# Kernel optimization log

Hardware: AMD Instinct MI355X
Metric: run time of the kernel (lower is better)

Reference implementation:

```python
import jax, jax.numpy as jnp
import numpy as np

K = 8               # top-k frequencies
PRED_LEN = 96       # prediction_length
LOW_FREQ = 1        # low_frequency cutoff (drops DC)


def setup_inputs() -> dict:
    key = jax.random.key(0)
    x = jax.random.normal(key, (32, 2048, 64), dtype=jnp.float32)
    return {"x": x}


def reference(x):
    b, t, d = x.shape
    x_freq = jnp.fft.rfft(x, axis=1)                 # (b, t//2+1, d) complex
    freqs = jnp.fft.rfftfreq(t).astype(x.dtype)
    if t % 2 == 0:
        x_freq = x_freq[:, LOW_FREQ:-1]              # drop DC and Nyquist
        f = freqs[LOW_FREQ:-1]
    else:
        x_freq = x_freq[:, LOW_FREQ:]
        f = freqs[LOW_FREQ:]

    # top-k over frequency dim (axis=1), independently per (b, d)
    mag = jnp.abs(x_freq)                            # (b, F, d)
    _, idx = jax.lax.top_k(jnp.moveaxis(mag, 1, 2), K)  # (b, d, K), sorted desc
    idx = jnp.moveaxis(idx, 1, 2)                    # (b, K, d)
    x_k = jnp.take_along_axis(x_freq, idx, axis=1)   # (b, K, d) complex
    f_k = f[idx]                                     # (b, K, d)

    # extrapolate: add conjugate (negative) frequencies, then cos-sum
    x2 = jnp.concatenate([x_k, jnp.conj(x_k)], axis=1)  # (b, 2K, d)
    f2 = jnp.concatenate([f_k, -f_k], axis=1)           # (b, 2K, d)
    t_val = jnp.arange(t + PRED_LEN, dtype=x.dtype)     # (T,)
    amp = jnp.abs(x2) / t                               # (b, 2K, d)
    phase = jnp.angle(x2)                               # (b, 2K, d)
    # (b, 2K, T, d) broadcast intermediate, reduced over freq axis
    x_time = amp[:, :, None, :] * jnp.cos(
        2.0 * np.float32(np.pi) * f2[:, :, None, :] * t_val[None, None, :, None]
        + phase[:, :, None, :]
    )
    return x_time.sum(axis=1)                        # (b, t+PRED_LEN, d)
```

## Files before the change

### kernel.cpp

```cpp
#include <hip/hip_runtime.h>
#include <math.h>

#define BB 32
#define TT 2048
#define DD 64
#define PRED 96
#define TP (TT + PRED)
#define KTOP 8
#define MARGIN 8e-4f
#define PI_D 3.14159265358979323846

__device__ __forceinline__ int br6(int l) { return (int)(__brev((unsigned)l) >> 26); }
static constexpr int BR3[8] = {0,4,2,6,1,5,3,7};
static constexpr float C32T[16] = {
    1.0f, 0.98078528040323044913f, 0.92387953251128675613f, 0.83146961230254523708f,
    0.70710678118654752440f, 0.55557023301960222474f, 0.38268343236508977173f, 0.19509032201612826785f,
    0.0f, -0.19509032201612826785f, -0.38268343236508977173f, -0.55557023301960222474f,
    -0.70710678118654752440f, -0.83146961230254523708f, -0.92387953251128675613f, -0.98078528040323044913f};
static constexpr float S32T[16] = {
    0.0f, 0.19509032201612826785f, 0.38268343236508977173f, 0.55557023301960222474f,
    0.70710678118654752440f, 0.83146961230254523708f, 0.92387953251128675613f, 0.98078528040323044913f,
    1.0f, 0.98078528040323044913f, 0.92387953251128675613f, 0.83146961230254523708f,
    0.70710678118654752440f, 0.55557023301960222474f, 0.38268343236508977173f, 0.19509032201612826785f};

__device__ __forceinline__ float2 ctw(float2 a, int m) {
    const float rev = (float)m * (1.0f / 2048.0f);
    const float c = __builtin_amdgcn_cosf(rev);
    const float s = __builtin_amdgcn_sinf(rev);
    return make_float2(a.x * c + a.y * s, a.y * c - a.x * s);
}

#define EXB(wvi,pi) ((wvi) * 1152 + (pi) * 18)
#define SRE(a) POOL[4608 + (a)]
#define SIM(a) POOL[6720 + (a)]

__global__ __launch_bounds__(256, 4) void fused_kernel(const float* __restrict__ x,
                                                       float* __restrict__ out) {
    __shared__ float POOL[8832];
    __shared__ int   coefK[2][KTOP];
    __shared__ float coefR[2][KTOP], coefI[2][KTOP];

    const int t    = threadIdx.x;
    const int wv   = t >> 6, p = t & 63;
    const int bid  = blockIdx.x;
    const int xcd  = bid & 7;
    const int idx  = bid >> 3;
    const int b    = ((idx >> 3) << 1) | (xcd >> 2);
    const int dp   = ((xcd & 3) << 3) | (idx & 7);

    const float2* xv = (const float2*)x;
    const size_t xbase = (size_t)b * TT * (DD / 2) + dp;
    const int br2wv = ((wv & 1) << 1) | ((wv >> 1) & 1);
    const int rl = 4 * br6(p) + br2wv;

    float2 v[8];
    #pragma unroll
    for (int i = 0; i < 8; ++i)
        v[i] = xv[xbase + (size_t)(256 * BR3[i] + rl) * (DD / 2)];

    #pragma unroll
    for (int s = 1; s <= 3; ++s) {
        const int m = 1 << s, half = m >> 1, stepw = 32 >> s;
        #pragma unroll
        for (int g = 0; g < 8; g += m) {
            #pragma unroll
            for (int j = 0; j < half; ++j) {
                const float c = C32T[j * stepw], sn = S32T[j * stepw];
                const int i0 = g + j, i1 = i0 + half;
                const float tr = c * v[i1].x + sn * v[i1].y;
                const float ti = c * v[i1].y - sn * v[i1].x;
                v[i1] = make_float2(v[i0].x - tr, v[i0].y - ti);
                v[i0] = make_float2(v[i0].x + tr, v[i0].y + ti);
            }
        }
    }

    #pragma unroll
    for (int q = 1; q < 8; ++q) v[q] = ctw(v[q], (rl * q) & (TT - 1));

    #pragma unroll
    for (int s = 1; s <= 6; ++s) {
        const int half = 1 << (s - 1);
        const float rev = (float)(p & (half - 1)) / (float)(1 << s);
        const float wc  = __builtin_amdgcn_cosf(rev);
        const float wsn = __builtin_amdgcn_sinf(rev);
        const bool  hi  = (p & half) != 0;
        #pragma unroll
        for (int q = 0; q < 8; ++q) {
            float2 pv;
            pv.x = __shfl_xor(v[q].x, half, 64);
            pv.y = __shfl_xor(v[q].y, half, 64);
            const float2 bsv = hi ? v[q] : pv;
            const float2 asv = hi ? pv : v[q];
            const float tr = wc * bsv.x + wsn * bsv.y;
            const float ti = wc * bsv.y - wsn * bsv.x;
            v[q] = hi ? make_float2(asv.x - tr, asv.y - ti)
                      : make_float2(asv.x + tr, asv.y + ti);
        }
    }

    {
        const int exw = EXB(wv, p);
        #pragma unroll
        for (int q = 0; q < 8; ++q) *(float2*)&POOL[exw + 2 * q] = v[q];
    }
    __syncthreads();
    {
        const int exr = EXB(wv ^ 1, p);
        const float rev7 = (float)p * (1.0f / 128.0f);
        const float c7 = __builtin_amdgcn_cosf(rev7);
        const float s7 = __builtin_amdgcn_sinf(rev7);
        const bool hi7 = (wv & 1) != 0;
        #pragma unroll
        for (int q = 0; q < 8; ++q) {
            const float2 pv = *(const float2*)&POOL[exr + 2 * q];
            const float2 bsv = hi7 ? v[q] : pv;
            const float2 asv = hi7 ? pv : v[q];
            const float tr = c7 * bsv.x + s7 * bsv.y;
            const float ti = c7 * bsv.y - s7 * bsv.x;
            v[q] = hi7 ? make_float2(asv.x - tr, asv.y - ti)
                       : make_float2(asv.x + tr, asv.y + ti);
        }
    }
    __syncthreads();

    {
        const int exw = EXB(wv, p);
        #pragma unroll
        for (int q = 0; q < 8; ++q) *(float2*)&POOL[exw + 2 * q] = v[q];
    }
    __syncthreads();
    {
        const int exr = EXB(wv ^ 2, p);
        const float rev8 = (float)(64 * (wv & 1) + p) * (1.0f / 256.0f);
        const float c8 = __builtin_amdgcn_cosf(rev8);
        const float s8 = __builtin_amdgcn_sinf(rev8);
        const bool hi8 = ((wv >> 1) & 1) != 0;
        const int kb = 512 * wv + 8 * p;
        #pragma unroll
        for (int q = 0; q < 8; ++q) {
            const float2 pv = *(const float2*)&POOL[exr + 2 * q];
            const float2 bsv = hi8 ? v[q] : pv;
            const float2 asv = hi8 ? pv : v[q];
            const float tr = c8 * bsv.x + s8 * bsv.y;
            const float ti = c8 * bsv.y - s8 * bsv.x;
            const float re = hi8 ? (asv.x - tr) : (asv.x + tr);
            const float im = hi8 ? (asv.y - ti) : (asv.y + ti);
            const int k = kb + q, a = k + (k >> 5);
            SRE(a) = re;
            SIM(a) = im;
        }
    }
    __syncthreads();

    if (wv < 2) {
        const int w = wv;
        unsigned A[16];
        #pragma unroll
        for (int q = 0; q < 16; ++q) {
            const int k = 16 * p + q;
            unsigned kk = 0u;
            if (k != 0) {
                const int a1 = k + (k >> 5);
                const int pk = TT - k, a2 = pk + (pk >> 5);
                const float zr = SRE(a1), zi = SIM(a1);
                const float yr = SRE(a2), yi = SIM(a2);
                float cr, ci;
                if (w == 0) { cr = 0.5f * (zr + yr); ci = 0.5f * (zi - yi); }
                else        { cr = 0.5f * (zi + yi); ci = 0.5f * (yr - zr); }
                const float mg = cr * cr + ci * ci;
                kk = (__float_as_uint(mg) & 0xFFFFF800u) | (unsigned)(2047 - k);
            }
            A[q] = kk;
        }

        #pragma unroll
        for (int sz = 2; sz <= 16; sz <<= 1) {
            #pragma unroll
            for (int d = sz >> 1; d > 0; d >>= 1) {
                #pragma unroll
                for (int i2 = 0; i2 < 16; ++i2) {
                    const int j2i = i2 ^ d;
                    if (j2i > i2) {
                        const bool desc = ((i2 & sz) == 0);
                        const unsigned a = A[i2], b2 = A[j2i];
                        const unsigned mx = a > b2 ? a : b2, mn = a > b2 ? b2 : a;
                        A[i2] = desc ? mx : mn;  A[j2i] = desc ? mn : mx;
                    }
                }
            }
        }
        #pragma unroll
        for (int off = 1; off <= 32; off <<= 1) {
            unsigned Bv[16];
            #pragma unroll
            for (int i2 = 0; i2 < 16; ++i2)
                Bv[i2] = (unsigned)__shfl_xor((int)A[i2], off, 64);
            #pragma unroll
            for (int i2 = 0; i2 < 16; ++i2) {
                const unsigned o = Bv[15 - i2];
                A[i2] = A[i2] > o ? A[i2] : o;
            }
            #pragma unroll
            for (int d = 8; d > 0; d >>= 1) {
                #pragma unroll
                for (int i2 = 0; i2 < 16; ++i2) {
                    if ((i2 & d) == 0) {
                        const int j2i = i2 + d;
                        const unsigned a = A[i2], b2 = A[j2i];
                        A[i2] = a > b2 ? a : b2;  A[j2i] = a > b2 ? b2 : a;
                    }
                }
            }
        }

        const float m8f = __uint_as_float(A[7] & 0xFFFFF800u);
        unsigned bandmask = 0u;
        #pragma unroll
        for (int r = 0; r < 16; ++r) {
            const float mr = __uint_as_float(A[r] & 0xFFFFF800u);
            if (fabsf(mr - m8f) <= MARGIN * m8f) bandmask |= (1u << r);
        }
        const int flg = (bandmask != (1u << 7)) ? 1 : 0;

        unsigned myk = 0u;
        #pragma unroll
        for (int i2 = 0; i2 < 16; ++i2) myk = (p == i2) ? A[i2] : myk;
        const int kcand = 2047 - (int)(myk & 0x7FFu);

        if (!flg && p < KTOP) {
            const int k = kcand, a1 = k + (k >> 5), pk = TT - k, a2 = pk + (pk >> 5);
            const float zr = SRE(a1), zi = SIM(a1);
            const float yr = SRE(a2), yi = SIM(a2);
            float cr, ci;
            if (w == 0) { cr = 0.5f * (zr + yr); ci = 0.5f * (zi - yi); }
            else        { cr = 0.5f * (zi + yi); ci = 0.5f * (yr - zr); }
            coefK[w][p] = k;
            coefR[w][p] = cr * (2.0f / (float)TT);
            coefI[w][p] = ci * (2.0f / (float)TT);
        }

        if (flg) {
            float sv[32];
            const float* xs = x + (size_t)b * TT * DD + 2 * dp + w;
            #pragma unroll
            for (int m2 = 0; m2 < 32; ++m2)
                sv[m2] = xs[(size_t)(p + 64 * m2) * DD];
            const double thA = -2.0 * PI_D * (double)p / 64.0;
            const double thB = -2.0 * PI_D * (double)p / (double)TT;
            const double wac = cos(thA), was = sin(thA);
            const double wbc = cos(thB), wbs = sin(thB);

            const unsigned bm = bandmask;
            const int lo = (int)__builtin_ctz(bm);
            double myM = 0.0, myR = 0.0, myI = 0.0;
            for (int r = 0; r < 16; ++r) {
                if (!((bm >> r) & 1u)) continue;
                const int kr = __shfl(kcand, r, 64);
                double ar = 0.0, ai = 0.0;
                for (int m2 = 0; m2 < 32; ++m2) {
                    const int n  = p + 64 * m2;
                    const int mm = (n * kr) & (TT - 1);
                    const double qc  = __shfl(wac, mm >> 5, 64);
                    const double qs  = __shfl(was, mm >> 5, 64);
                    const double rc2 = __shfl(wbc, mm & 31, 64);
                    const double rs2 = __shfl(wbs, mm & 31, 64);
                    const double wr = qc * rc2 - qs * rs2;
                    const double wi = qc * rs2 + qs * rc2;
                    ar = fma((double)sv[m2], wr, ar);
                    ai = fma((double)sv[m2], wi, ai);
                }
                #pragma unroll
                for (int off = 32; off; off >>= 1) {
                    ar += __shfl_xor(ar, off, 64);
                    ai += __shfl_xor(ai, off, 64);
                }
                if (p == r) { myM = ar * ar + ai * ai; myR = ar; myI = ai; }
            }
            const int h16 = p & 15;
            const double selfM = __shfl(myM, h16, 64);
            const int    selfK = __shfl(kcand, h16, 64);
            int rb = 0;
            for (int r2 = 0; r2 < 16; ++r2) {
                if (!((bm >> r2) & 1u)) continue;
                const double om = __shfl(myM, r2, 64);
                const int    ok = __shfl(kcand, r2, 64);
                if (r2 != h16 && (om > selfM || (om == selfM && ok < selfK))) ++rb;
            }
            const int isband = (int)((bm >> h16) & 1u);
            const int rank = isband ? (lo + rb) : h16;
            if (p < 16 && rank < KTOP) {
                coefK[w][rank] = kcand;
                if (isband) {
                    coefR[w][rank] = (float)(myR * (2.0 / (double)TT));
                    coefI[w][rank] = (float)(myI * (2.0 / (double)TT));
                } else {
                    const int k = kcand, a1 = k + (k >> 5), pk = TT - k, a2 = pk + (pk >> 5);
                    const float zr = SRE(a1), zi = SIM(a1);
                    const float yr = SRE(a2), yi = SIM(a2);
                    float cr, ci;
                    if (w == 0) { cr = 0.5f * (zr + yr); ci = 0.5f * (zi - yi); }
                    else        { cr = 0.5f * (zi + yi); ci = 0.5f * (yr - zr); }
                    coefR[w][rank] = cr * (2.0f / (float)TT);
                    coefI[w][rank] = ci * (2.0f / (float)TT);
                }
            }
        }
    }
    __syncthreads();

    const int d2 = t & 1, tq = t >> 1;
    int   kc[KTOP];
    float fr[KTOP], fi[KTOP], pc[KTOP], ps[KTOP], rc[KTOP], rs[KTOP];
    #pragma unroll
    for (int pp = 0; pp < KTOP; ++pp) {
        kc[pp] = coefK[d2][pp];
        fr[pp] = coefR[d2][pp];
        fi[pp] = coefI[d2][pp];
        const int j0 = (kc[pp] * tq) & (TT - 1);
        const float rv0 = (float)j0 * (1.0f / 2048.0f);
        pc[pp] = __builtin_amdgcn_cosf(rv0);
        ps[pp] = __builtin_amdgcn_sinf(rv0);
        const int jr = (kc[pp] * 128) & (TT - 1);
        const float rvr = (float)jr * (1.0f / 2048.0f);
        rc[pp] = __builtin_amdgcn_cosf(rvr);
        rs[pp] = __builtin_amdgcn_sinf(rvr);
    }
    float* ob = out + (size_t)b * TP * DD + 2 * dp + d2;
    #pragma unroll 2
    for (int m = 0; m < 17; ++m) {
        const int tv = tq + 128 * m;
        float acc = 0.0f;
        #pragma unroll
        for (int pp = 0; pp < KTOP; ++pp) acc += fr[pp] * pc[pp] - fi[pp] * ps[pp];
        if (tv < TP) ob[(size_t)tv * DD] = acc;
        #pragma unroll
        for (int pp = 0; pp < KTOP; ++pp) {
            const float nc = pc[pp] * rc[pp] - ps[pp] * rs[pp];
            const float ns = pc[pp] * rs[pp] + ps[pp] * rc[pp];
            pc[pp] = nc; ps[pp] = ns;
        }
    }
}

extern "C" void kernel_launch(void* const* d_in, const int* in_sizes, int n_in,
                              void* d_out, int out_size, void* d_ws, size_t ws_size,
                              hipStream_t stream) {
    const float* x = (const float*)d_in[0];
    float* out = (float*)d_out;
    (void)d_ws; (void)ws_size; (void)in_sizes; (void)n_in; (void)out_size;

    fused_kernel<<<BB * 32, 256, 0, stream>>>(x, out);
}
```

Baseline: 98.85 us.

## Pre-transpose input into per-channel-pair contiguous workspace before fused FFT kernel

Adds a separate transpose kernel that rewrites x from (b, t, d) into a workspace laid out per (b, channel pair) with time contiguous as float2. The fused FFT/top-k kernel then reads its inputs and fallback samples from contiguous rows instead of strided 256-byte-apart loads. This aims to cut poorly coalesced global reads, at the cost of an extra kernel launch and a full extra read and write of the input (16 MB each way). It only runs when a large enough workspace is provided; otherwise the old path is used.

```diff
diff --git a/kernel.cpp b/kernel.cpp
--- a/kernel.cpp
+++ b/kernel.cpp
@@ -9,6 +9,7 @@
 #define KTOP 8
 #define MARGIN 8e-4f
 #define PI_D 3.14159265358979323846
+#define XT2_BYTES ((size_t)BB * 32 * TT * sizeof(float2))
 
 __device__ __forceinline__ int br6(int l) { return (int)(__brev((unsigned)l) >> 26); }
 static constexpr int BR3[8] = {0,4,2,6,1,5,3,7};
@@ -30,11 +31,48 @@
     return make_float2(a.x * c + a.y * s, a.y * c - a.x * s);
 }
 
+__global__ __launch_bounds__(256) void transpose_kernel(const float* __restrict__ x,
+                                                        float2* __restrict__ xt2) {
+    __shared__ float tl[64 * 68];
+    const int tid = threadIdx.x;
+    const int bid = blockIdx.x;
+    const int b   = bid >> 5;
+    const int t0  = (bid & 31) * 64;
+
+    const float4* xr = (const float4*)(x + ((size_t)b * TT + t0) * DD);
+    {
+        const int r = tid >> 2, c = tid & 3;
+        #pragma unroll
+        for (int j = 0; j < 4; ++j) {
+            const float4 f = xr[r * 16 + c + 4 * j];
+            *(float4*)&tl[r * 68 + (c + 4 * j) * 4] = f;
+        }
+    }
+    __syncthreads();
+
+    {
+        const int dp = tid >> 3, c = tid & 7;
+        float2* orow = xt2 + ((size_t)b * 32 + dp) * TT + t0;
+        #pragma unroll
+        for (int j = 0; j < 4; ++j) {
+            const int t = 16 * j + 2 * c;
+            float4 o;
+            o.x = tl[t * 68 + 2 * dp];
+            o.y = tl[t * 68 + 2 * dp + 1];
+            o.z = tl[(t + 1) * 68 + 2 * dp];
+            o.w = tl[(t + 1) * 68 + 2 * dp + 1];
+            *(float4*)&orow[t] = o;
+        }
+    }
+}
+
 #define EXB(wvi,pi) ((wvi) * 1152 + (pi) * 18)
 #define SRE(a) POOL[4608 + (a)]
 #define SIM(a) POOL[6720 + (a)]
 
+template<bool XT>
 __global__ __launch_bounds__(256, 4) void fused_kernel(const float* __restrict__ x,
+                                                       const float2* __restrict__ xt2,
                                                        float* __restrict__ out) {
     __shared__ float POOL[8832];
     __shared__ int   coefK[2][KTOP];
@@ -48,6 +86,7 @@
     const int b    = ((idx >> 3) << 1) | (xcd >> 2);
     const int dp   = ((xcd & 3) << 3) | (idx & 7);
 
+    const float2* xp = XT ? (xt2 + ((size_t)b * 32 + dp) * TT) : (const float2*)0;
     const float2* xv = (const float2*)x;
     const size_t xbase = (size_t)b * TT * (DD / 2) + dp;
     const int br2wv = ((wv & 1) << 1) | ((wv >> 1) & 1);
@@ -55,8 +94,10 @@
 
     float2 v[8];
     #pragma unroll
-    for (int i = 0; i < 8; ++i)
-        v[i] = xv[xbase + (size_t)(256 * BR3[i] + rl) * (DD / 2)];
+    for (int i = 0; i < 8; ++i) {
+        const int n = 256 * BR3[i] + rl;
+        v[i] = XT ? xp[n] : xv[xbase + (size_t)n * (DD / 2)];
+    }
 
     #pragma unroll
     for (int s = 1; s <= 3; ++s) {
@@ -242,10 +283,16 @@
 
         if (flg) {
             float sv[32];
-            const float* xs = x + (size_t)b * TT * DD + 2 * dp + w;
-            #pragma unroll
-            for (int m2 = 0; m2 < 32; ++m2)
-                sv[m2] = xs[(size_t)(p + 64 * m2) * DD];
+            #pragma unroll
+            for (int m2 = 0; m2 < 32; ++m2) {
+                if (XT) {
+                    const float2 s2 = xp[p + 64 * m2];
+                    sv[m2] = (w == 0) ? s2.x : s2.y;
+                } else {
+                    const float* xs = x + (size_t)b * TT * DD + 2 * dp + w;
+                    sv[m2] = xs[(size_t)(p + 64 * m2) * DD];
+                }
+            }
             const double thA = -2.0 * PI_D * (double)p / 64.0;
             const double thB = -2.0 * PI_D * (double)p / (double)TT;
             const double wac = cos(thA), was = sin(thA);
@@ -348,7 +395,13 @@
                               hipStream_t stream) {
     const float* x = (const float*)d_in[0];
     float* out = (float*)d_out;
-    (void)d_ws; (void)ws_size; (void)in_sizes; (void)n_in; (void)out_size;
-
-    fused_kernel<<<BB * 32, 256, 0, stream>>>(x, out);
+    (void)in_sizes; (void)n_in; (void)out_size;
+
+    if (d_ws != nullptr && ws_size >= XT2_BYTES) {
+        float2* xt2 = (float2*)d_ws;
+        transpose_kernel<<<BB * 32, 256, 0, stream>>>(x, xt2);
+        fused_kernel<true><<<BB * 32, 256, 0, stream>>>(x, xt2, out);
+    } else {
+        fused_kernel<false><<<BB * 32, 256, 0, stream>>>(x, nullptr, out);
+    }
 }
```

Result: slower. 103.7 us (+4.9%).
